# Performance work log

Hardware: AMD Instinct MI355X
Metric: run time of the kernel (lower is better)

## Reference

```python
import jax, jax.numpy as jnp
import numpy as np

B, S, D_MODEL = 2, 2048, 2048
N_HEADS, N_KV = 32, 8
HEAD_DIM = D_MODEL // N_HEADS          # 64
HPG = N_HEADS // N_KV                  # heads per group = 4
DIM_K = HEAD_DIM * N_KV                # 512 (used as softmax scale per original code)


def setup_inputs() -> dict:
    key = jax.random.key(0)
    ks = jax.random.split(key, 11)
    s = lambda fan_in: 1.0 / np.sqrt(fan_in)
    return {
        "inputs_q": jax.random.normal(ks[0], (B, S, D_MODEL), jnp.float32),
        "inputs_k": jax.random.normal(ks[1], (B, S, D_MODEL), jnp.float32),
        "inputs_v": jax.random.normal(ks[2], (B, S, D_MODEL), jnp.float32),
        "Wq": jax.random.normal(ks[3], (D_MODEL, D_MODEL), jnp.float32) * s(D_MODEL),
        "bq": jnp.zeros((D_MODEL,), jnp.float32),
        "Wk": jax.random.normal(ks[4], (D_MODEL, DIM_K), jnp.float32) * s(D_MODEL),
        "bk": jnp.zeros((DIM_K,), jnp.float32),
        "Wv": jax.random.normal(ks[5], (D_MODEL, DIM_K), jnp.float32) * s(D_MODEL),
        "bv": jnp.zeros((DIM_K,), jnp.float32),
        "Wo": jax.random.normal(ks[6], (D_MODEL, D_MODEL), jnp.float32) * s(D_MODEL),
        "bo": jnp.zeros((D_MODEL,), jnp.float32),
    }


def reference(inputs_q, inputs_k, inputs_v, Wq, bq, Wk, bk, Wv, bv, Wo, bo):
    b, s, _ = inputs_q.shape
    q = inputs_q @ Wq + bq                       # [B,S,dim_q]
    k = inputs_k @ Wk + bk                       # [B,S,dim_k]
    v = inputs_v @ Wv + bv                       # [B,S,dim_v]
    q = q.reshape(b, s, N_KV, HPG, HEAD_DIM)     # b m g p d
    k = k.reshape(b, s, N_KV, HEAD_DIM)          # b n g d
    v = v.reshape(b, s, N_KV, HEAD_DIM)          # b n g d
    # logits[b,g,p,m,n] = q . k ; scale by sqrt(dim_k) per original code
    logits = jnp.einsum('bmgpd,bngd->bgpmn', q, k) / jnp.sqrt(jnp.float32(DIM_K))
    # causal mask (lower triangular allowed)
    causal = jnp.tril(jnp.ones((s, s), bool))
    logits = jnp.where(causal, logits, -jnp.inf)
    attn = jax.nn.softmax(logits, axis=-1)       # [B,G,P,M,N]
    out = jnp.einsum('bgpmn,bngd->bmgpd', attn, v)
    out = out.reshape(b, s, N_KV * HPG * HEAD_DIM)
    return out @ Wo + bo
```

## Files before the change

kernel.cpp:

```cpp
#include <hip/hip_runtime.h>
#include <hip/hip_bf16.h>

typedef __hip_bfloat16 bf16;
typedef float f32x4 __attribute__((ext_vector_type(4)));
typedef float f32x16 __attribute__((ext_vector_type(16)));
typedef short bf16x8 __attribute__((ext_vector_type(8)));

#define B_   2
#define S_   2048
#define DM   2048
#define HD   64
#define NH   32

__device__ __forceinline__ void async16(void* lds, const void* g) {
  __builtin_amdgcn_global_load_lds(
      (const __attribute__((address_space(1))) unsigned int*)g,
      (__attribute__((address_space(3))) unsigned int*)lds, 16, 0, 0);
}

template <int N> __device__ __forceinline__ void waitvm() {
  asm volatile("s_waitcnt vmcnt(%0)" :: "i"(N) : "memory");
}

__device__ __forceinline__ float exp2a(float x) {
  float r; asm("v_exp_f32 %0, %1" : "=v"(r) : "v"(x)); return r;
}
__device__ __forceinline__ unsigned cvtpk(float lo, float hi) {
  unsigned r; asm("v_cvt_pk_bf16_f32 %0, %1, %2" : "=v"(r) : "v"(lo), "v"(hi)); return r;
}
__device__ __forceinline__ void perm32swap(unsigned &a, unsigned &b) {
  asm volatile("v_permlane32_swap_b32 %0, %1" : "+v"(a), "+v"(b));
}

__global__ __launch_bounds__(256)
void prep_kernel(const float* __restrict__ xq, const float* __restrict__ xk,
                 const float* __restrict__ xv,
                 const float* __restrict__ Wq, const float* __restrict__ Wo,
                 const float* __restrict__ Wk, const float* __restrict__ Wv,
                 const float* __restrict__ bk, const float* __restrict__ bv,
                 bf16* __restrict__ Xq, bf16* __restrict__ Xk, bf16* __restrict__ Xv,
                 bf16* __restrict__ WqT, bf16* __restrict__ WoT, bf16* __restrict__ WkvT,
                 float* __restrict__ bkv) {
  const int blk = blockIdx.x;
  const int tid = threadIdx.x;

  if (blk < 12288) {
    const int a = blk >> 12;
    const int r = blk & 4095;
    const float* in = (a == 0) ? xq : (a == 1) ? xk : xv;
    bf16* out = (a == 0) ? Xq : (a == 1) ? Xk : Xv;
    const size_t i = ((size_t)r * 256 + tid) * 8;
    float4 v0 = *(const float4*)(in + i);
    float4 v1 = *(const float4*)(in + i + 4);
    union { bf16 h[8]; uint4 v; } u;
    u.h[0] = __float2bfloat16(v0.x); u.h[1] = __float2bfloat16(v0.y);
    u.h[2] = __float2bfloat16(v0.z); u.h[3] = __float2bfloat16(v0.w);
    u.h[4] = __float2bfloat16(v1.x); u.h[5] = __float2bfloat16(v1.y);
    u.h[6] = __float2bfloat16(v1.z); u.h[7] = __float2bfloat16(v1.w);
    *(uint4*)(out + i) = u.v;
    return;
  }

  int t = blk - 12288;
  const float* W; bf16* Wt; int N;
  if (t < 4096)       { W = Wq; Wt = WqT; N = 2048; }
  else if (t < 8192)  { t -= 4096; W = Wo; Wt = WoT; N = 2048; }
  else if (t < 9216)  { t -= 8192; W = Wk; Wt = WkvT; N = 512; }
  else if (t < 10240) { t -= 9216; W = Wv; Wt = WkvT + (size_t)512 * 2048; N = 512; }
  else {
    #pragma unroll
    for (int j = 0; j < 4; ++j) {
      const int i = tid * 4 + j;
      bkv[i] = (i < 512) ? bk[i] : bv[i - 512];
    }
    return;
  }
  const int k0 = (t & 63) * 32, n0 = (t >> 6) * 32;
  __shared__ float tile[32][33];
  const int tx = tid & 31, ty = tid >> 5;
  #pragma unroll
  for (int i = 0; i < 32; i += 8)
    tile[ty + i][tx] = W[(size_t)(k0 + ty + i) * N + n0 + tx];
  __syncthreads();
  #pragma unroll
  for (int i = 0; i < 32; i += 8)
    Wt[(size_t)(n0 + ty + i) * 2048 + k0 + tx] = __float2bfloat16(tile[tx][ty + i]);
}

__device__ __forceinline__ void store_out(float* C, size_t idx, float v) { C[idx] = v; }
__device__ __forceinline__ void store_out(bf16* C, size_t idx, float v) { C[idx] = __float2bfloat16(v); }

template <typename OUT>
__device__ __forceinline__ void gemm_body(const bf16* __restrict__ Au,
                                          const bf16* __restrict__ Bt,
                                          const float* __restrict__ bias, float omul,
                                          OUT* __restrict__ C, int N, int m0, int n0,
                                          bf16* As, bf16* Bs) {
  constexpr int BK = 32;
  const int tid = threadIdx.x;
  const int wave = tid >> 6, lane = tid & 63;
  const int l15 = lane & 15, l4 = lane >> 4;
  const int wm = (wave & 1) * 64, wn = (wave >> 1) * 64;

  f32x4 acc[4][4] = {};
  const int nk = 2048 / BK;

  auto stage = [&](int kt, int buf) {
    const int k0 = kt * BK;
    #pragma unroll
    for (int i = 0; i < 2; ++i) {
      const int rb = wave * 32 + i * 16;
      const int r  = rb + (lane >> 2);
      const int cs = (lane & 3) ^ ((r >> 1) & 3);
      async16(As + buf * 4096 + rb * BK, Au + (size_t)(m0 + r) * 2048 + k0 + cs * 8);
      async16(Bs + buf * 4096 + rb * BK, Bt + (size_t)(n0 + r) * 2048 + k0 + cs * 8);
    }
  };

  stage(0, 0);
  asm volatile("s_waitcnt vmcnt(0)" ::: "memory");
  __syncthreads();

  for (int kt = 0; kt < nk; ++kt) {
    const int cur = kt & 1;
    if (kt + 1 < nk) stage(kt + 1, cur ^ 1);
    bf16x8 af[4], bfr[4];
    #pragma unroll
    for (int f = 0; f < 4; ++f) {
      const int mr = wm + f * 16 + l15;
      af[f]  = *(const bf16x8*)(As + cur * 4096 + mr * BK + (l4 ^ ((mr >> 1) & 3)) * 8);
      const int nr = wn + f * 16 + l15;
      bfr[f] = *(const bf16x8*)(Bs + cur * 4096 + nr * BK + (l4 ^ ((nr >> 1) & 3)) * 8);
    }
    __builtin_amdgcn_s_setprio(1);
    #pragma unroll
    for (int i = 0; i < 4; ++i)
      #pragma unroll
      for (int j = 0; j < 4; ++j)
        acc[i][j] = __builtin_amdgcn_mfma_f32_16x16x32_bf16(af[i], bfr[j], acc[i][j], 0, 0, 0);
    __builtin_amdgcn_s_setprio(0);
    asm volatile("s_waitcnt vmcnt(0)" ::: "memory");
    __syncthreads();
  }

  const int r0 = m0 + wm + l4 * 4;
  const int c0 = n0 + wn + l15;
  #pragma unroll
  for (int j = 0; j < 4; ++j) {
    const int col = c0 + j * 16;
    const float bb = bias[col];
    #pragma unroll
    for (int i = 0; i < 4; ++i)
      #pragma unroll
      for (int r = 0; r < 4; ++r)
        store_out(C, (size_t)(r0 + i * 16 + r) * N + col, (acc[i][j][r] + bb) * omul);
  }
}

__device__ __forceinline__ void gemm256_body(const bf16* __restrict__ Au,
                                             const bf16* __restrict__ Bt,
                                             const float* __restrict__ bias, float omul,
                                             bf16* __restrict__ C, int N, int m0, int n0,
                                             char* smem) {
  char* AsB = smem;
  char* BsB = smem + 65536;
  const int tid = threadIdx.x;
  const int wave = tid >> 6, lane = tid & 63;
  const int l15 = lane & 15, l4 = lane >> 4;
  const int wr = wave >> 2, wc = wave & 3;

  f32x4 acc[8][4] = {};

  auto stage = [&](int buf, int kt) {
    const int k0 = kt * 64;
    #pragma unroll
    for (int i = 0; i < 4; ++i) {
      const int rb = wave * 32 + i * 8;
      const int r = rb + (lane >> 3);
      const int cs = (lane & 7) ^ (r & 7);
      async16(AsB + buf * 32768 + rb * 128, Au + (size_t)(m0 + r) * 2048 + k0 + cs * 8);
      async16(BsB + buf * 32768 + rb * 128, Bt + (size_t)(n0 + r) * 2048 + k0 + cs * 8);
    }
  };

  stage(0, 0);
  waitvm<0>();
  __builtin_amdgcn_s_barrier();
  asm volatile("" ::: "memory");

  for (int kt = 0; kt < 32; ++kt) {
    const int cur = kt & 1;
    if (kt + 1 < 32) stage(cur ^ 1, kt + 1);
    const char* ab = AsB + cur * 32768;
    const char* bb = BsB + cur * 32768;
    #pragma unroll
    for (int ks = 0; ks < 2; ++ks) {
      bf16x8 af[8], bg[4];
      #pragma unroll
      for (int mf = 0; mf < 8; ++mf) {
        const int row = wr * 128 + mf * 16 + l15;
        af[mf] = *(const bf16x8*)(ab + row * 128 + (((ks * 4 + l4) ^ (row & 7)) << 4));
      }
      #pragma unroll
      for (int nf = 0; nf < 4; ++nf) {
        const int row = wc * 64 + nf * 16 + l15;
        bg[nf] = *(const bf16x8*)(bb + row * 128 + (((ks * 4 + l4) ^ (row & 7)) << 4));
      }
      __builtin_amdgcn_s_setprio(1);
      #pragma unroll
      for (int mf = 0; mf < 8; ++mf)
        #pragma unroll
        for (int nf = 0; nf < 4; ++nf)
          acc[mf][nf] = __builtin_amdgcn_mfma_f32_16x16x32_bf16(af[mf], bg[nf],
                                                                acc[mf][nf], 0, 0, 0);
      __builtin_amdgcn_s_setprio(0);
    }
    waitvm<0>();
    __builtin_amdgcn_s_barrier();
    asm volatile("" ::: "memory");
  }

  const int r0 = m0 + wr * 128 + l4 * 4;
  const int c0 = n0 + wc * 64 + l15;
  #pragma unroll
  for (int nf = 0; nf < 4; ++nf) {
    const int col = c0 + nf * 16;
    const float bb2 = bias[col];
    #pragma unroll
    for (int mf = 0; mf < 8; ++mf)
      #pragma unroll
      for (int r = 0; r < 4; ++r)
        C[(size_t)(r0 + mf * 16 + r) * N + col] =
            __float2bfloat16((acc[mf][nf][r] + bb2) * omul);
  }
}

__global__ __launch_bounds__(512, 2)
void gemm_qkv(const bf16* __restrict__ Xq, const bf16* __restrict__ Xk,
              const bf16* __restrict__ Xv,
              const bf16* __restrict__ WqT, const bf16* __restrict__ WkvT,
              const float* __restrict__ bq, const float* __restrict__ bkv,
              bf16* __restrict__ Qb, bf16* __restrict__ KVb) {
  __shared__ __align__(16) char smem[131072];
  const int bid = blockIdx.x;
  const int wgid = (bid & 7) * 24 + (bid >> 3);
  const int m0 = (wgid & 15) * 256;
  const int ng = wgid >> 4;
  if (ng < 8) {
    gemm256_body(Xq, WqT, bq, 0.063758717f, Qb, 2048, m0, ng * 256, smem);
  } else {
    const int n0 = (ng - 8) * 256;
    gemm256_body(n0 < 512 ? Xk : Xv, WkvT, bkv, 1.0f, KVb, 1024, m0, n0, smem);
  }
}

__global__ __launch_bounds__(256)
void gemm_o(const bf16* __restrict__ AO, const bf16* __restrict__ WoT,
            const float* __restrict__ bo, float* __restrict__ out) {
  __shared__ __align__(16) bf16 As[2][128 * 32];
  __shared__ __align__(16) bf16 Bs[2][128 * 32];
  gemm_body<float>(AO, WoT, bo, 1.0f, out, 2048,
                   blockIdx.x * 128, blockIdx.y * 128, &As[0][0], &Bs[0][0]);
}

__global__ __launch_bounds__(256, 3)
void attn_kernel(const bf16* __restrict__ Q, const bf16* __restrict__ KV, bf16* __restrict__ O) {
  const int h = blockIdx.x & 31, b = blockIdx.x >> 5;
  const int qt = 15 - blockIdx.y;
  const int g = h >> 2;
  const int tid = threadIdx.x;
  const int wave = tid >> 6, lane = tid & 63;
  const int l31 = lane & 31, l5 = lane >> 5;

  __shared__ __align__(16) char smem[40960];
  bf16* KsBuf = (bf16*)smem;
  bf16* VtBuf = (bf16*)(smem + 24576);
  char* ob = smem + wave * 4608;

  const bf16* KVb = KV + (size_t)(b * S_) * 1024;
  const int kcol = g * HD;
  const int vcol = 512 + g * HD;
  const int kv2 = tid & 31, vd0 = (tid >> 5) * 8;

  auto stageK = [&](int buf, int kv0) {
    #pragma unroll
    for (int i2 = 0; i2 < 2; ++i2) {
      const int rb = wave * 16 + i2 * 8;
      const int r = rb + (lane >> 3);
      const int cs = (lane & 7) ^ (r & 7);
      async16(KsBuf + buf * 4096 + rb * 64, KVb + (size_t)(kv0 + r) * 1024 + kcol + cs * 8);
    }
  };
  auto writeV = [&](int buf, uint4 va, uint4 vb) {
    const unsigned short* a0 = (const unsigned short*)&va;
    const unsigned short* a1 = (const unsigned short*)&vb;
    char* base = (char*)VtBuf + buf * 8192;
    #pragma unroll
    for (int j = 0; j < 8; ++j) {
      unsigned val = (unsigned)a0[j] | ((unsigned)a1[j] << 16);
      const int d = vd0 + j;
      *(unsigned*)(base + d * 128 + ((kv2 * 4) ^ ((d & 7) << 4))) = val;
    }
  };

  const int qbase = qt * 128;
  const int nt = 2 * qt + 2;
  const int qrow = qbase + wave * 32 + l31;
  const int wmax = qbase + wave * 32 + 31;

  bf16x8 qf[4];
  const bf16* qp = Q + (size_t)(b * S_ + qrow) * DM + h * HD + l5 * 8;
  #pragma unroll
  for (int ks = 0; ks < 4; ++ks) qf[ks] = *(const bf16x8*)(qp + ks * 16);

  f32x16 ot[2] = {};
  float m = -3.0e38f, lsum = 0.f;
  uint4 vr0, vr1;

  {
    const bf16* vp = KVb + (size_t)(2 * kv2) * 1024 + vcol + vd0;
    vr0 = *(const uint4*)vp;
    vr1 = *(const uint4*)(vp + 1024);
  }
  stageK(0, 0);
  stageK(1, 64);
  waitvm<4>();
  writeV(0, vr0, vr1);
  waitvm<2>();
  asm volatile("s_waitcnt lgkmcnt(0)" ::: "memory");
  __builtin_amdgcn_s_barrier();
  asm volatile("" ::: "memory");

  for (int t = 0; t < nt; ++t) {
    const int kv0 = t * 64;
    if (t + 1 < nt) {
      const bf16* vp = KVb + (size_t)((t + 1) * 64 + 2 * kv2) * 1024 + vcol + vd0;
      vr0 = *(const uint4*)vp;
      vr1 = *(const uint4*)(vp + 1024);
    }
    if (t + 2 < nt) stageK((t + 2) % 3, (t + 2) * 64);

    if (kv0 <= wmax) {
      const char* kb = (const char*)(KsBuf + (t % 3) * 4096);
      const char* vb = (const char*)(VtBuf + (t & 1) * 4096);
      f32x16 sT[2] = {};
      __builtin_amdgcn_s_setprio(1);
      #pragma unroll
      for (int ks = 0; ks < 4; ++ks) {
        #pragma unroll
        for (int i = 0; i < 2; ++i) {
          const int row = i * 32 + l31;
          bf16x8 kf = *(const bf16x8*)(kb + row * 128 +
                                       ((ks * 32 + l5 * 16) ^ ((row & 7) << 4)));
          sT[i] = __builtin_amdgcn_mfma_f32_32x32x16_bf16(kf, qf[ks], sT[i], 0, 0, 0);
        }
      }
      __builtin_amdgcn_s_setprio(0);
      if (kv0 + 63 > qbase + wave * 32) {
        #pragma unroll
        for (int i = 0; i < 2; ++i)
          #pragma unroll
          for (int r = 0; r < 16; ++r) {
            const int kvg = kv0 + i * 32 + ((r & 3) + 8 * (r >> 2)) + 4 * l5;
            if (kvg > qrow) sT[i][r] = -3.0e38f;
          }
      }
      float a16[16];
      #pragma unroll
      for (int r = 0; r < 16; ++r) a16[r] = fmaxf(sT[0][r], sT[1][r]);
      #pragma unroll
      for (int s2 = 8; s2 >= 1; s2 >>= 1)
        #pragma unroll
        for (int r = 0; r < 8; ++r) if (r < s2) a16[r] = fmaxf(a16[r], a16[r + s2]);
      float pm = fmaxf(a16[0], __shfl_xor(a16[0], 32));
      if (!__all(pm - m <= 8.f)) {
        const float mn = fmaxf(m, pm);
        const float alpha = exp2a(m - mn);
        m = mn;
        lsum *= alpha;
        #pragma unroll
        for (int r = 0; r < 16; ++r) { ot[0][r] *= alpha; ot[1][r] *= alpha; }
      }
      float rs0 = 0.f, rs1 = 0.f;
      unsigned pk[2][8];
      #pragma unroll
      for (int i = 0; i < 2; ++i)
        #pragma unroll
        for (int rr = 0; rr < 8; ++rr) {
          const float p0 = exp2a(sT[i][2 * rr] - m);
          const float p1 = exp2a(sT[i][2 * rr + 1] - m);
          if (i == 0) rs0 += p0 + p1; else rs1 += p0 + p1;
          pk[i][rr] = cvtpk(p0, p1);
        }
      float rs = rs0 + rs1;
      rs += __shfl_xor(rs, 32);
      lsum += rs;
      #pragma unroll
      for (int i = 0; i < 2; ++i) {
        #pragma unroll
        for (int kp = 0; kp < 2; ++kp) {
          unsigned w0 = pk[i][4 * kp + 0], w1 = pk[i][4 * kp + 1];
          unsigned w2 = pk[i][4 * kp + 2], w3 = pk[i][4 * kp + 3];
          perm32swap(w0, w2);
          perm32swap(w1, w3);
          union { unsigned u[4]; bf16x8 v; } pf = {{w0, w1, w2, w3}};
          const int ks2 = i * 2 + kp;
          __builtin_amdgcn_s_setprio(1);
          #pragma unroll
          for (int f = 0; f < 2; ++f) {
            const int row = f * 32 + l31;
            bf16x8 vf = *(const bf16x8*)(vb + row * 128 +
                                         ((ks2 * 32 + l5 * 16) ^ ((row & 7) << 4)));
            ot[f] = __builtin_amdgcn_mfma_f32_32x32x16_bf16(vf, pf.v, ot[f], 0, 0, 0);
          }
          __builtin_amdgcn_s_setprio(0);
        }
      }
    }

    if (t + 2 < nt) waitvm<2>();
    else            waitvm<0>();
    if (t + 1 < nt) writeV((t + 1) & 1, vr0, vr1);
    asm volatile("s_waitcnt lgkmcnt(0)" ::: "memory");
    __builtin_amdgcn_s_barrier();
    asm volatile("" ::: "memory");
  }

  const float inv = 1.0f / lsum;
  #pragma unroll
  for (int f = 0; f < 2; ++f)
    #pragma unroll
    for (int g2 = 0; g2 < 4; ++g2) {
      uint2 val;
      val.x = cvtpk(ot[f][g2 * 4 + 0] * inv, ot[f][g2 * 4 + 1] * inv);
      val.y = cvtpk(ot[f][g2 * 4 + 2] * inv, ot[f][g2 * 4 + 3] * inv);
      *(uint2*)(ob + l31 * 144 + f * 64 + g2 * 16 + l5 * 8) = val;
    }
  asm volatile("s_waitcnt lgkmcnt(0)" ::: "memory");
  __builtin_amdgcn_sched_barrier(0);
  #pragma unroll
  for (int rr = 0; rr < 4; ++rr) {
    const int row = rr * 8 + (lane >> 3);
    uint4 dv = *(const uint4*)(ob + row * 144 + (lane & 7) * 16);
    *(uint4*)(O + (size_t)(b * S_ + qbase + wave * 32 + row) * DM + h * HD + (lane & 7) * 8) = dv;
  }
}

extern "C" void kernel_launch(void* const* d_in, const int* in_sizes, int n_in,
                              void* d_out, int out_size, void* d_ws, size_t ws_size,
                              hipStream_t stream) {
  const float* xq = (const float*)d_in[0];
  const float* xk = (const float*)d_in[1];
  const float* xv = (const float*)d_in[2];
  const float* Wq = (const float*)d_in[3];
  const float* bq = (const float*)d_in[4];
  const float* Wk = (const float*)d_in[5];
  const float* bk = (const float*)d_in[6];
  const float* Wv = (const float*)d_in[7];
  const float* bv = (const float*)d_in[8];
  const float* Wo = (const float*)d_in[9];
  const float* bo = (const float*)d_in[10];
  float* out = (float*)d_out;

  char* ws = (char*)d_ws;
  bf16*  Xq   = (bf16*)(ws);
  bf16*  Xk   = (bf16*)(ws + 16777216);
  bf16*  Xv   = (bf16*)(ws + 33554432);
  bf16*  WqT  = (bf16*)(ws + 50331648);
  bf16*  WkvT = (bf16*)(ws + 58720256);
  bf16*  WoT  = (bf16*)(ws + 62914560);
  float* bkv  = (float*)(ws + 71303168);
  bf16*  Qb   = (bf16*)(ws + 71307264);
  bf16*  KVb  = (bf16*)(ws + 88084480);
  bf16*  AO   = Xq;

  prep_kernel<<<22529, 256, 0, stream>>>(xq, xk, xv, Wq, Wo, Wk, Wv, bk, bv,
                                         Xq, Xk, Xv, WqT, WoT, WkvT, bkv);
  gemm_qkv<<<192, 512, 0, stream>>>(Xq, Xk, Xv, WqT, WkvT, bq, bkv, Qb, KVb);
  attn_kernel<<<dim3(64, 16), 256, 0, stream>>>(Qb, KVb, AO);
  gemm_o<<<dim3(32, 16), 256, 0, stream>>>(AO, WoT, bo, out);
}
```

Baseline: 210.0 us.

## Compute softmax row sums via MFMA and reorder causal tile schedule

The per-tile row-sum reduction (VALU adds plus a cross-lane shuffle) is replaced by an extra MFMA that multiplies the probability fragment by a ones vector, accumulating the denominator in matrix-core accumulators. The grid is also flattened to 1D with a zig-zag mapping of query tiles (heavy, then ascending, then descending, then light) to balance causal work across waves of blocks. This trades VALU work for one more MFMA per k-step and extra accumulator registers, which may affect occupancy at three blocks per SM.

```diff
diff --git a/kernel.cpp b/kernel.cpp
--- a/kernel.cpp
+++ b/kernel.cpp
@@ -265,8 +265,15 @@
 
 __global__ __launch_bounds__(256, 3)
 void attn_kernel(const bf16* __restrict__ Q, const bf16* __restrict__ KV, bf16* __restrict__ O) {
-  const int h = blockIdx.x & 31, b = blockIdx.x >> 5;
-  const int qt = 15 - blockIdx.y;
+  const int bi = blockIdx.x;
+  const int w = bi >> 8, c = bi & 255;
+  const int grp = c >> 6, hb = c & 63;
+  int qt;
+  if (w == 0)      qt = 15 - grp;
+  else if (w == 1) qt = 8 + grp;
+  else if (w == 2) qt = 7 - grp;
+  else             qt = grp;
+  const int h = hb & 31, b = hb >> 5;
   const int g = h >> 2;
   const int tid = threadIdx.x;
   const int wave = tid >> 6, lane = tid & 63;
@@ -313,8 +320,15 @@
   #pragma unroll
   for (int ks = 0; ks < 4; ++ks) qf[ks] = *(const bf16x8*)(qp + ks * 16);
 
+  union { unsigned u[4]; bf16x8 v; } ones;
+  {
+    const unsigned ov = (l31 == 0) ? 0x3F803F80u : 0u;
+    ones.u[0] = ov; ones.u[1] = ov; ones.u[2] = ov; ones.u[3] = ov;
+  }
+
   f32x16 ot[2] = {};
-  float m = -3.0e38f, lsum = 0.f;
+  f32x16 ot2 = {};
+  float m = -3.0e38f;
   uint4 vr0, vr1;
 
   {
@@ -377,11 +391,10 @@
         const float mn = fmaxf(m, pm);
         const float alpha = exp2a(m - mn);
         m = mn;
-        lsum *= alpha;
+        ot2[0] *= alpha;
         #pragma unroll
         for (int r = 0; r < 16; ++r) { ot[0][r] *= alpha; ot[1][r] *= alpha; }
       }
-      float rs0 = 0.f, rs1 = 0.f;
       unsigned pk[2][8];
       #pragma unroll
       for (int i = 0; i < 2; ++i)
@@ -389,12 +402,8 @@
         for (int rr = 0; rr < 8; ++rr) {
           const float p0 = exp2a(sT[i][2 * rr] - m);
           const float p1 = exp2a(sT[i][2 * rr + 1] - m);
-          if (i == 0) rs0 += p0 + p1; else rs1 += p0 + p1;
           pk[i][rr] = cvtpk(p0, p1);
         }
-      float rs = rs0 + rs1;
-      rs += __shfl_xor(rs, 32);
-      lsum += rs;
       #pragma unroll
       for (int i = 0; i < 2; ++i) {
         #pragma unroll
@@ -413,6 +422,7 @@
                                          ((ks2 * 32 + l5 * 16) ^ ((row & 7) << 4)));
             ot[f] = __builtin_amdgcn_mfma_f32_32x32x16_bf16(vf, pf.v, ot[f], 0, 0, 0);
           }
+          ot2 = __builtin_amdgcn_mfma_f32_32x32x16_bf16(ones.v, pf.v, ot2, 0, 0, 0);
           __builtin_amdgcn_s_setprio(0);
         }
       }
@@ -426,6 +436,7 @@
     asm volatile("" ::: "memory");
   }
 
+  const float lsum = ot2[0] + __shfl_xor(ot2[0], 32);
   const float inv = 1.0f / lsum;
   #pragma unroll
   for (int f = 0; f < 2; ++f)
@@ -477,6 +488,6 @@
   prep_kernel<<<22529, 256, 0, stream>>>(xq, xk, xv, Wq, Wo, Wk, Wv, bk, bv,
                                          Xq, Xk, Xv, WqT, WoT, WkvT, bkv);
   gemm_qkv<<<192, 512, 0, stream>>>(Xq, Xk, Xv, WqT, WkvT, bq, bkv, Qb, KVb);
-  attn_kernel<<<dim3(64, 16), 256, 0, stream>>>(Qb, KVb, AO);
+  attn_kernel<<<1024, 256, 0, stream>>>(Qb, KVb, AO);
   gemm_o<<<dim3(32, 16), 256, 0, stream>>>(AO, WoT, bo, out);
 }
```

After: 208.4 us. About the same (-0.8%).
